# Optimization experiments

Hardware: AMD Instinct MI355X
Metric: run time of the kernel (lower is better)

## Reference

```python
import jax, jax.numpy as jnp
import numpy as np
import math

MIN_NORM = 1e-15


def artanh(x):
    # torch Artanh.forward: clamp then 0.5*(log(1+x)-log(1-x))
    xc = jnp.clip(x, -0.99 + 1e-07, 0.99 - 1e-07)
    return 0.5 * (jnp.log1p(xc) - jnp.log1p(-xc))


def logmap0(p, c):
    p = jnp.nan_to_num(p, nan=0.0)
    sqrt_c = c ** 0.5
    p_norm = jnp.maximum(jnp.linalg.norm(p, axis=-1, keepdims=True), MIN_NORM)
    arg = jnp.clip(sqrt_c * p_norm, -0.99, 0.99)
    scale = (1.0 / sqrt_c) * artanh(arg) / p_norm
    return jnp.clip(scale * p, -50.0, 50.0)


def expmap0(u, c):
    sqrt_c = c ** 0.5
    u_norm = jnp.maximum(jnp.linalg.norm(u, axis=-1, keepdims=True), MIN_NORM)
    return jnp.tanh(sqrt_c * u_norm) * u / (sqrt_c * u_norm)


def proj(x, c):
    eps = 1e-10
    x_norm = jnp.linalg.norm(x, axis=-1, keepdims=True)
    bad = jnp.isnan(x_norm) | jnp.isinf(x_norm)
    x_norm = jnp.where(bad, 0.0, x_norm)
    max_norm = 1.0 / math.sqrt(c) - eps
    safe_norm = jnp.maximum(x_norm, 1e-09)
    return jnp.where(x_norm > max_norm, x * (max_norm / safe_norm), x)


def mobius_matvec(m, x, c):
    # stabilize zero rows of m: add 1e-6 to column 0 of rows with tiny norm
    row_norms = jnp.linalg.norm(m, axis=1)
    m = m.at[:, 0].add(jnp.where(row_norms < 1e-08, 1e-06, 0.0))
    x_tan = logmap0(x, c)                       # [N, d_in]
    mx = jnp.clip(x_tan @ m.T, -1000.0, 1000.0)  # [N, d_out]
    return proj(expmap0(mx, c), c)


def setup_inputs() -> dict:
    key = jax.random.key(0)
    k1, k2 = jax.random.split(key)
    x = jax.random.normal(k1, (65536, 1024), dtype=jnp.float32)
    m = jax.random.normal(k2, (1024, 1024), dtype=jnp.float32)
    return {"x": x, "m": m}


def reference(x, m):
    return mobius_matvec(m, x, 1.0)
```

## Files before the change

kernel.cpp:

```cpp
#include <hip/hip_runtime.h>
#include <cstdint>
#include <cstddef>

typedef unsigned short u16;
typedef __bf16 bf16x8 __attribute__((ext_vector_type(8)));
typedef float f32x4 __attribute__((ext_vector_type(4)));

__device__ __forceinline__ u16 f2bf(float f) {
  uint32_t u = __builtin_bit_cast(uint32_t, f);
  u += 0x7FFFu + ((u >> 16) & 1u);
  return (u16)(u >> 16);
}
__device__ __forceinline__ float bf2f(u16 h) {
  return __builtin_bit_cast(float, (uint32_t)h << 16);
}

__global__ __launch_bounds__(256) void k_logmap0(const float* __restrict__ x,
                                                 u16* __restrict__ xt) {
  const size_t row = blockIdx.x;
  float4 v = ((const float4*)(x + row * 1024))[threadIdx.x];
  float ss = v.x * v.x + v.y * v.y + v.z * v.z + v.w * v.w;
#pragma unroll
  for (int off = 32; off > 0; off >>= 1) ss += __shfl_down(ss, off, 64);
  __shared__ float wsum[4];
  if ((threadIdx.x & 63) == 0) wsum[threadIdx.x >> 6] = ss;
  __syncthreads();
  float tot = wsum[0] + wsum[1] + wsum[2] + wsum[3];
  float n = fmaxf(sqrtf(tot), 1e-15f);
  float arg = fminf(n, 0.99f);
  float xc = fminf(fmaxf(arg, -0.99f + 1e-7f), 0.99f - 1e-7f);
  float at = 0.5f * (log1pf(xc) - log1pf(-xc));
  float scale = at / n;
  ushort4 o;
  o.x = f2bf(fminf(fmaxf(scale * v.x, -50.f), 50.f));
  o.y = f2bf(fminf(fmaxf(scale * v.y, -50.f), 50.f));
  o.z = f2bf(fminf(fmaxf(scale * v.z, -50.f), 50.f));
  o.w = f2bf(fminf(fmaxf(scale * v.w, -50.f), 50.f));
  ((ushort4*)(xt + row * 1024))[threadIdx.x] = o;
}

__global__ __launch_bounds__(256) void k_cvt_m(const float* __restrict__ m,
                                               u16* __restrict__ mb) {
  int i = blockIdx.x * 256 + threadIdx.x;
  float4 v = ((const float4*)m)[i];
  ushort4 o;
  o.x = f2bf(v.x); o.y = f2bf(v.y); o.z = f2bf(v.z); o.w = f2bf(v.w);
  ((ushort4*)mb)[i] = o;
}

__global__ __launch_bounds__(256) void k_gemm_bt(const u16* __restrict__ A,
                                                 const u16* __restrict__ B,
                                                 u16* __restrict__ C,
                                                 int Kdim) {
  __shared__ alignas(16) u16 As[128 * 32];
  __shared__ alignas(16) u16 Bs[128 * 32];
  const int tid = threadIdx.x;
  const int lane = tid & 63;
  const int wave = tid >> 6;
  const size_t row0 = (size_t)blockIdx.x * 128;
  const int col0 = blockIdx.y * 128;
  const int wm = (wave & 1) * 64;
  const int wn = (wave >> 1) * 64;

  const int s_row = tid >> 2;
  const int s_k = (tid & 3) * 8;
  const u16* aP = A + (row0 + s_row) * (size_t)Kdim + s_k;
  const u16* bP = B + (size_t)(col0 + s_row) * Kdim + s_k;
  const size_t rstep = (size_t)64 * Kdim;
  u16* AsW0 = As + wave * 512;
  u16* AsW1 = As + 2048 + wave * 512;
  u16* BsW0 = Bs + wave * 512;
  u16* BsW1 = Bs + 2048 + wave * 512;

  const int frow = lane & 15;
  const int fk = (lane >> 4) * 8;
  const u16* aF = As + (wm + frow) * 32 + fk;
  const u16* bF = Bs + (wn + frow) * 32 + fk;

  f32x4 acc[4][4];
#pragma unroll
  for (int i = 0; i < 4; ++i)
#pragma unroll
    for (int j = 0; j < 4; ++j) {
      f32x4 z = {0.f, 0.f, 0.f, 0.f};
      acc[i][j] = z;
    }

  for (int k0 = 0; k0 < Kdim; k0 += 32) {
    __syncthreads();
    __builtin_amdgcn_global_load_lds(
        (const __attribute__((address_space(1))) void*)(aP + k0),
        (__attribute__((address_space(3))) void*)AsW0, 16, 0, 0);
    __builtin_amdgcn_global_load_lds(
        (const __attribute__((address_space(1))) void*)(aP + k0 + rstep),
        (__attribute__((address_space(3))) void*)AsW1, 16, 0, 0);
    __builtin_amdgcn_global_load_lds(
        (const __attribute__((address_space(1))) void*)(bP + k0),
        (__attribute__((address_space(3))) void*)BsW0, 16, 0, 0);
    __builtin_amdgcn_global_load_lds(
        (const __attribute__((address_space(1))) void*)(bP + k0 + rstep),
        (__attribute__((address_space(3))) void*)BsW1, 16, 0, 0);
    __syncthreads();

    bf16x8 af[4], bfr[4];
#pragma unroll
    for (int i = 0; i < 4; ++i) af[i] = *(const bf16x8*)(aF + i * 512);
#pragma unroll
    for (int j = 0; j < 4; ++j) bfr[j] = *(const bf16x8*)(bF + j * 512);
#pragma unroll
    for (int i = 0; i < 4; ++i)
#pragma unroll
      for (int j = 0; j < 4; ++j)
        acc[i][j] = __builtin_amdgcn_mfma_f32_16x16x32_bf16(af[i], bfr[j],
                                                            acc[i][j], 0, 0, 0);
  }

#pragma unroll
  for (int i = 0; i < 4; ++i) {
    size_t rb = row0 + wm + i * 16 + (lane >> 4) * 4;
#pragma unroll
    for (int j = 0; j < 4; ++j) {
      int cc = col0 + wn + j * 16 + (lane & 15);
#pragma unroll
      for (int r = 0; r < 4; ++r) {
        float v = fminf(fmaxf(acc[i][j][r], -1000.f), 1000.f);
        C[(rb + r) * 1024 + cc] = f2bf(v);
      }
    }
  }
}

__global__ __launch_bounds__(256) void k_expmap_proj(const u16* __restrict__ mx,
                                                     float* __restrict__ out) {
  const size_t row = blockIdx.x;
  ushort4 q = ((const ushort4*)(mx + row * 1024))[threadIdx.x];
  float u0 = bf2f(q.x), u1 = bf2f(q.y), u2 = bf2f(q.z), u3 = bf2f(q.w);
  float ss = u0 * u0 + u1 * u1 + u2 * u2 + u3 * u3;
#pragma unroll
  for (int off = 32; off > 0; off >>= 1) ss += __shfl_down(ss, off, 64);
  __shared__ float wsum[4];
  if ((threadIdx.x & 63) == 0) wsum[threadIdx.x >> 6] = ss;
  __syncthreads();
  float tot = wsum[0] + wsum[1] + wsum[2] + wsum[3];
  float n = fmaxf(sqrtf(tot), 1e-15f);
  float t = tanhf(n);
  float scale = t / n;
  float ynorm = t;
  const float max_norm = 1.0f - 1e-10f;
  if (ynorm > max_norm) scale *= max_norm / fmaxf(ynorm, 1e-9f);
  float4 o;
  o.x = scale * u0; o.y = scale * u1; o.z = scale * u2; o.w = scale * u3;
  ((float4*)(out + row * 1024))[threadIdx.x] = o;
}

extern "C" void kernel_launch(void* const* d_in, const int* in_sizes, int n_in,
                              void* d_out, int out_size, void* d_ws, size_t ws_size,
                              hipStream_t stream) {
  const float* x = (const float*)d_in[0];
  const float* m = (const float*)d_in[1];
  float* out = (float*)d_out;
  const int K = 1024, N = 1024;
  const int M = in_sizes[0] / K;

  u16* mb = (u16*)d_ws;
  u16* mx = (u16*)d_ws + (size_t)N * K;
  u16* xt = (u16*)d_out;

  k_logmap0<<<M, 256, 0, stream>>>(x, xt);
  k_cvt_m<<<(N * K / 4) / 256, 256, 0, stream>>>(m, mb);
  dim3 g(M / 128, N / 128);
  k_gemm_bt<<<g, 256, 0, stream>>>(xt, mb, mx, K);
  k_expmap_proj<<<M, 256, 0, stream>>>(mx, out);
}
```

Baseline: 679.0 us.

## Use one wave per row in norm kernels, swizzle GEMM tiles, vectorize C stores

The logmap0 and expmap_proj kernels now give each row to a single wave, so the norm is reduced with xor-shuffles alone and the shared-memory reduction and __syncthreads are gone. The GEMM grid becomes a 1-D launch with a grouped tile swizzle, so groups of 8 row panels sweep all 8 column tiles together for better L2 reuse of A and B. The MFMA operands are swapped so each lane holds four consecutive output columns, which lets the epilogue write 8-byte ushort4 stores instead of scattered 2-byte stores. Together these target the small strided C writes and sync overhead, at the cost of a new tile mapping that has to cover the output correctly.

```diff
diff --git a/kernel.cpp b/kernel.cpp
--- a/kernel.cpp
+++ b/kernel.cpp
@@ -17,26 +17,33 @@
 
 __global__ __launch_bounds__(256) void k_logmap0(const float* __restrict__ x,
                                                  u16* __restrict__ xt) {
-  const size_t row = blockIdx.x;
-  float4 v = ((const float4*)(x + row * 1024))[threadIdx.x];
-  float ss = v.x * v.x + v.y * v.y + v.z * v.z + v.w * v.w;
+  const int wave = threadIdx.x >> 6, lane = threadIdx.x & 63;
+  const size_t row = (size_t)blockIdx.x * 4 + wave;
+  const float4* xr = (const float4*)(x + row * 1024);
+  float4 v[4];
 #pragma unroll
-  for (int off = 32; off > 0; off >>= 1) ss += __shfl_down(ss, off, 64);
-  __shared__ float wsum[4];
-  if ((threadIdx.x & 63) == 0) wsum[threadIdx.x >> 6] = ss;
-  __syncthreads();
-  float tot = wsum[0] + wsum[1] + wsum[2] + wsum[3];
-  float n = fmaxf(sqrtf(tot), 1e-15f);
+  for (int j = 0; j < 4; ++j) v[j] = xr[lane + j * 64];
+  float ss = 0.f;
+#pragma unroll
+  for (int j = 0; j < 4; ++j)
+    ss += v[j].x * v[j].x + v[j].y * v[j].y + v[j].z * v[j].z + v[j].w * v[j].w;
+#pragma unroll
+  for (int off = 32; off > 0; off >>= 1) ss += __shfl_xor(ss, off, 64);
+  float n = fmaxf(sqrtf(ss), 1e-15f);
   float arg = fminf(n, 0.99f);
   float xc = fminf(fmaxf(arg, -0.99f + 1e-7f), 0.99f - 1e-7f);
   float at = 0.5f * (log1pf(xc) - log1pf(-xc));
   float scale = at / n;
-  ushort4 o;
-  o.x = f2bf(fminf(fmaxf(scale * v.x, -50.f), 50.f));
-  o.y = f2bf(fminf(fmaxf(scale * v.y, -50.f), 50.f));
-  o.z = f2bf(fminf(fmaxf(scale * v.z, -50.f), 50.f));
-  o.w = f2bf(fminf(fmaxf(scale * v.w, -50.f), 50.f));
-  ((ushort4*)(xt + row * 1024))[threadIdx.x] = o;
+  ushort4* xo = (ushort4*)(xt + row * 1024);
+#pragma unroll
+  for (int j = 0; j < 4; ++j) {
+    ushort4 o;
+    o.x = f2bf(fminf(fmaxf(scale * v[j].x, -50.f), 50.f));
+    o.y = f2bf(fminf(fmaxf(scale * v[j].y, -50.f), 50.f));
+    o.z = f2bf(fminf(fmaxf(scale * v[j].z, -50.f), 50.f));
+    o.w = f2bf(fminf(fmaxf(scale * v[j].w, -50.f), 50.f));
+    xo[lane + j * 64] = o;
+  }
 }
 
 __global__ __launch_bounds__(256) void k_cvt_m(const float* __restrict__ m,
@@ -57,8 +64,11 @@
   const int tid = threadIdx.x;
   const int lane = tid & 63;
   const int wave = tid >> 6;
-  const size_t row0 = (size_t)blockIdx.x * 128;
-  const int col0 = blockIdx.y * 128;
+  const int id = blockIdx.x;
+  const int panel = ((id >> 6) << 3) | (id & 7);
+  const int ntile = (id >> 3) & 7;
+  const size_t row0 = (size_t)panel * 128;
+  const int col0 = ntile * 128;
   const int wm = (wave & 1) * 64;
   const int wn = (wave >> 1) * 64;
 
@@ -111,46 +121,59 @@
     for (int i = 0; i < 4; ++i)
 #pragma unroll
       for (int j = 0; j < 4; ++j)
-        acc[i][j] = __builtin_amdgcn_mfma_f32_16x16x32_bf16(af[i], bfr[j],
+        acc[i][j] = __builtin_amdgcn_mfma_f32_16x16x32_bf16(bfr[j], af[i],
                                                             acc[i][j], 0, 0, 0);
   }
 
 #pragma unroll
   for (int i = 0; i < 4; ++i) {
-    size_t rb = row0 + wm + i * 16 + (lane >> 4) * 4;
+    size_t r = row0 + wm + i * 16 + (lane & 15);
+    u16* Crow = C + r * 1024 + col0 + wn + (lane >> 4) * 4;
 #pragma unroll
     for (int j = 0; j < 4; ++j) {
-      int cc = col0 + wn + j * 16 + (lane & 15);
-#pragma unroll
-      for (int r = 0; r < 4; ++r) {
-        float v = fminf(fmaxf(acc[i][j][r], -1000.f), 1000.f);
-        C[(rb + r) * 1024 + cc] = f2bf(v);
-      }
+      ushort4 o;
+      o.x = f2bf(fminf(fmaxf(acc[i][j][0], -1000.f), 1000.f));
+      o.y = f2bf(fminf(fmaxf(acc[i][j][1], -1000.f), 1000.f));
+      o.z = f2bf(fminf(fmaxf(acc[i][j][2], -1000.f), 1000.f));
+      o.w = f2bf(fminf(fmaxf(acc[i][j][3], -1000.f), 1000.f));
+      *(ushort4*)(Crow + j * 16) = o;
     }
   }
 }
 
 __global__ __launch_bounds__(256) void k_expmap_proj(const u16* __restrict__ mx,
                                                      float* __restrict__ out) {
-  const size_t row = blockIdx.x;
-  ushort4 q = ((const ushort4*)(mx + row * 1024))[threadIdx.x];
-  float u0 = bf2f(q.x), u1 = bf2f(q.y), u2 = bf2f(q.z), u3 = bf2f(q.w);
-  float ss = u0 * u0 + u1 * u1 + u2 * u2 + u3 * u3;
+  const int wave = threadIdx.x >> 6, lane = threadIdx.x & 63;
+  const size_t row = (size_t)blockIdx.x * 4 + wave;
+  const ushort4* mr = (const ushort4*)(mx + row * 1024);
+  ushort4 q[4];
 #pragma unroll
-  for (int off = 32; off > 0; off >>= 1) ss += __shfl_down(ss, off, 64);
-  __shared__ float wsum[4];
-  if ((threadIdx.x & 63) == 0) wsum[threadIdx.x >> 6] = ss;
-  __syncthreads();
-  float tot = wsum[0] + wsum[1] + wsum[2] + wsum[3];
-  float n = fmaxf(sqrtf(tot), 1e-15f);
+  for (int j = 0; j < 4; ++j) q[j] = mr[lane + j * 64];
+  float u[16];
+#pragma unroll
+  for (int j = 0; j < 4; ++j) {
+    u[j * 4 + 0] = bf2f(q[j].x); u[j * 4 + 1] = bf2f(q[j].y);
+    u[j * 4 + 2] = bf2f(q[j].z); u[j * 4 + 3] = bf2f(q[j].w);
+  }
+  float ss = 0.f;
+#pragma unroll
+  for (int e = 0; e < 16; ++e) ss += u[e] * u[e];
+#pragma unroll
+  for (int off = 32; off > 0; off >>= 1) ss += __shfl_xor(ss, off, 64);
+  float n = fmaxf(sqrtf(ss), 1e-15f);
   float t = tanhf(n);
   float scale = t / n;
   float ynorm = t;
   const float max_norm = 1.0f - 1e-10f;
   if (ynorm > max_norm) scale *= max_norm / fmaxf(ynorm, 1e-9f);
-  float4 o;
-  o.x = scale * u0; o.y = scale * u1; o.z = scale * u2; o.w = scale * u3;
-  ((float4*)(out + row * 1024))[threadIdx.x] = o;
+  float4* orow = (float4*)(out + row * 1024);
+#pragma unroll
+  for (int j = 0; j < 4; ++j) {
+    float4 o;
+    o.x = scale * u[j * 4 + 0]; o.y = scale * u[j * 4 + 1];
+    o.z = scale * u[j * 4 + 2]; o.w = scale * u[j * 4 + 3];
+    orow[lane + j * 64] = o;
+  }
 }
 
 extern "C" void kernel_launch(void* const* d_in, const int* in_sizes, int n_in,
@@ -166,9 +189,8 @@
   u16* mx = (u16*)d_ws + (size_t)N * K;
   u16* xt = (u16*)d_out;
 
-  k_logmap0<<<M, 256, 0, stream>>>(x, xt);
+  k_logmap0<<<M / 4, 256, 0, stream>>>(x, xt);
   k_cvt_m<<<(N * K / 4) / 256, 256, 0, stream>>>(m, mb);
-  dim3 g(M / 128, N / 128);
-  k_gemm_bt<<<g, 256, 0, stream>>>(xt, mb, mx, K);
-  k_expmap_proj<<<M, 256, 0, stream>>>(mx, out);
+  k_gemm_bt<<<(M / 128) * (N / 128), 256, 0, stream>>>(xt, mb, mx, K);
+  k_expmap_proj<<<M / 4, 256, 0, stream>>>(mx, out);
 }
```

After: 689.5 us. About the same (+1.6%).
